# Performance work log

Measured on AMD Instinct MI355X. Metric: run time of the kernel, lower is better.

Reference implementation:

```python
import math
import jax, jax.numpy as jnp
import numpy as np

H, PQ, PV, E, C, S, N = 12, 4, 8, 16, 128, 384, 512


def setup_inputs() -> dict:
    key = jax.random.key(0)
    ks = jax.random.split(key, 16)
    rn = lambda k, shape, scale=1.0: jax.random.normal(k, shape, jnp.float32) * scale
    single = rn(ks[0], (N, S))
    pair = rn(ks[1], (N, N, C))
    R, _ = jnp.linalg.qr(rn(ks[2], (N, 3, 3)))  # proper orthonormal frames
    t = rn(ks[3], (N, 3))
    w = 0.02
    return dict(
        single_representation=single,
        pair_representation=pair,
        rotations=R,
        translations=t,
        Wq=rn(ks[4], (H, S, E), w),
        Wk=rn(ks[5], (H, S, E), w),
        Wv=rn(ks[6], (H, S, E), w),
        Wqp=rn(ks[7], (H, PQ, S, 3), w),
        Wkp=rn(ks[8], (H, PQ, S, 3), w),
        Wvp=rn(ks[9], (H, PV, S, 3), w),
        Wb=rn(ks[10], (H, C), w),
        Wout=rn(ks[11], (H * (C + E + PV * 4), S), w),
        b_out=jnp.zeros((S,), jnp.float32),
        scale_head=jnp.ones((H,), jnp.float32),
    )


def _frame_apply(R, t, pts):
    # R:[N,3,3], t:[N,3], pts:[H,P,N,3] -> R_n @ p + t_n per residue n
    return jnp.einsum('nij,hpnj->hpni', R, pts) + t[None, None, :, :]


def reference(single_representation, pair_representation, rotations, translations,
              Wq, Wk, Wv, Wqp, Wkp, Wvp, Wb, Wout, b_out, scale_head):
    single, pair = single_representation, pair_representation
    n = single.shape[0]

    # --- sequence QK term ---
    q = jnp.einsum('nd,hde->hne', single, Wq)
    k = jnp.einsum('nd,hde->hne', single, Wk)
    w_single = math.sqrt(1.0 / E) * jnp.einsum('hne,hme->hnm', q, k)  # [H,N,N]

    # --- pair bias term ---
    w_pair = jnp.einsum('nmc,hc->hnm', pair, Wb)  # [H,N,N]

    # --- frame (3D point distance) term ---
    qp = jnp.einsum('nd,hpdk->hpnk', single, Wqp)  # [H,PQ,N,3]
    kp = jnp.einsum('nd,hpdk->hpnk', single, Wkp)
    lqp = _frame_apply(rotations, translations, qp)
    lkp = _frame_apply(rotations, translations, kp)
    diff = lqp[:, :, :, None, :] - lkp[:, :, None, :, :]   # [H,PQ,N,N,3]
    sqd = jnp.sum(diff * diff, axis=(1, 4))                 # [H,N,N] (sum over points & xyz)
    w_frame = (-math.sqrt(1.0 / (18 * PQ))) * jax.nn.softplus(scale_head)[:, None, None] * sqd

    w = jax.nn.softmax(w_single + w_pair + w_frame, axis=-1)  # [H,N,N]

    # --- sequence value aggregation ---
    v = jnp.einsum('nd,hde->hne', single, Wv)
    att_single = jnp.einsum('hnm,hme->hne', w, v)             # [H,N,E]
    att_single = jnp.transpose(att_single, (1, 0, 2)).reshape(n, -1)

    # --- pair value aggregation (faithful to source: sums over query index too) ---
    colsum = jnp.sum(w, axis=1)                               # [H,N] = sum_a w[h,a,b]
    att_pair = jnp.einsum('hb,ibc->hic', colsum, pair)        # [H,N,C]
    att_pair = jnp.transpose(att_pair, (1, 0, 2)).reshape(n, -1)

    # --- 3D point value aggregation ---
    vp = jnp.einsum('nd,hpdk->hpnk', single, Wvp)             # [H,PV,N,3]
    lvp = _frame_apply(rotations, translations, vp)
    local_out = jnp.einsum('hnm,hpmk->hpnk', w, lvp)          # [H,PV,N,3]
    Rinv = jnp.swapaxes(rotations, -1, -2)                    # R^T
    tinv = -jnp.einsum('nij,nj->ni', Rinv, translations)      # -R^T t
    global_out = _frame_apply(Rinv, tinv, local_out)          # [H,PV,N,3]
    out_points = jnp.transpose(global_out, (2, 1, 0, 3)).reshape(n, -1)  # [N, PV*H*3]
    out_norm = jnp.linalg.norm(global_out, axis=-1)           # [H,PV,N]
    out_norm = jnp.transpose(out_norm, (2, 1, 0)).reshape(n, -1)         # [N, PV*H]

    att = jnp.concatenate([att_single, att_pair, out_points, out_norm], axis=-1)
    return att @ Wout + b_out
```

## Files before the change

### kernel.cpp

```cpp
#include <hip/hip_runtime.h>
#include <math.h>

#define NRES 512
#define HH 12
#define PQn 4
#define PVn 8
#define En 16
#define Cn 128
#define Sn 384
#define ATT_COLS 2112

#define OFF_Q    0
#define OFF_K    (OFF_Q   + HH*NRES*En)
#define OFF_V    (OFF_K   + HH*NRES*En)
#define OFF_LQP  (OFF_V   + HH*NRES*En)
#define OFF_LKP  (OFF_LQP + HH*NRES*12)
#define OFF_LVP  (OFF_LKP + HH*NRES*12)
#define OFF_CS   (OFF_LVP + HH*NRES*24)
#define OFF_ATT  (OFF_CS  + NRES*HH)
#define OFF_LG   (OFF_ATT + NRES*ATT_COLS)
#define OFF_PART OFF_LG
#define OFF_KC   OFF_ATT
#define OFF_D1   (OFF_KC + NRES*HH*28)
#define OFF_D0   (OFF_D1 + NRES*HH)
#define KSPLIT 16
#define KCHUNK (ATT_COLS/KSPLIT)
#define OROWS 8
#define NGRP 2

__global__ __launch_bounds__(256) void ipa_proj(
    const float* __restrict__ single, const float* __restrict__ Rm,
    const float* __restrict__ tr,
    const float* __restrict__ Wq, const float* __restrict__ Wk,
    const float* __restrict__ Wv, const float* __restrict__ Wqp,
    const float* __restrict__ Wkp, const float* __restrict__ Wvp,
    float* __restrict__ ws)
{
  float* q   = ws + OFF_Q;  float* k   = ws + OFF_K;  float* v   = ws + OFF_V;
  float* lqp = ws + OFF_LQP; float* lkp = ws + OFF_LKP; float* lvp = ws + OFF_LVP;
  const int n0 = blockIdx.x * 8;
  const int g  = blockIdx.y;
  const int tid = threadIdx.x;
  __shared__ float sS[8][388];
  __shared__ float sR[8][9];
  __shared__ float sT[8][3];
  #pragma unroll
  for (int i = 0; i < 3; ++i) {
    int idx = i*256 + tid;
    int r = idx / 96, c4 = idx % 96;
    float4 val = *reinterpret_cast<const float4*>(single + (size_t)(n0 + r)*Sn + c4*4);
    *reinterpret_cast<float4*>(&sS[r][c4*4]) = val;
  }
  if (tid < 72)      sR[tid/9][tid%9] = Rm[(size_t)(n0 + tid/9)*9 + tid%9];
  else if (tid < 96) { int r = (tid-72)/3; sT[r][(tid-72)%3] = tr[(size_t)(n0+r)*3 + (tid-72)%3]; }
  __syncthreads();
  #pragma unroll
  for (int i = 0; i < 3; ++i) {
    int item = i*256 + tid;
    int nl = item & 7;
    int ul = item >> 3;
    int u  = g*96 + ul;
    const float* srow = sS[nl];
    if (u < 576) {
      int which = u/192, r = u%192, h = r>>4, e = r&15;
      const float* W = (which==0 ? Wq : which==1 ? Wk : Wv) + (size_t)h*Sn*En + e;
      float acc = 0.f;
      #pragma unroll 8
      for (int d = 0; d < Sn; ++d) acc = fmaf(srow[d], W[(size_t)d*En], acc);
      float* dst = (which==0 ? q : which==1 ? k : v);
      dst[((size_t)h*NRES + (n0+nl))*En + e] = acc;
    } else {
      int u2 = u - 576;
      const float* W; float* dst;
      if (u2 < 48)      { int h=u2>>2,     p=u2&3;      W = Wqp + (size_t)(h*PQn+p)*Sn*3; dst = lqp + ((size_t)h*NRES + (n0+nl))*12 + p*3; }
      else if (u2 < 96) { int h=(u2-48)>>2,p=(u2-48)&3; W = Wkp + (size_t)(h*PQn+p)*Sn*3; dst = lkp + ((size_t)h*NRES + (n0+nl))*12 + p*3; }
      else              { int h=(u2-96)>>3,p=(u2-96)&7; W = Wvp + (size_t)(h*PVn+p)*Sn*3; dst = lvp + ((size_t)h*NRES + (n0+nl))*24 + p*3; }
      float x0=0.f,x1=0.f,x2=0.f;
      #pragma unroll 4
      for (int d = 0; d < Sn; ++d) {
        float sv = srow[d];
        x0 = fmaf(sv, W[d*3+0], x0);
        x1 = fmaf(sv, W[d*3+1], x1);
        x2 = fmaf(sv, W[d*3+2], x2);
      }
      const float* R8 = sR[nl]; const float* T8 = sT[nl];
      dst[0] = R8[0]*x0 + R8[1]*x1 + R8[2]*x2 + T8[0];
      dst[1] = R8[3]*x0 + R8[4]*x1 + R8[5]*x2 + T8[1];
      dst[2] = R8[6]*x0 + R8[7]*x1 + R8[8]*x2 + T8[2];
    }
  }
}

__global__ __launch_bounds__(256) void ipa_pack(
    const float* __restrict__ scale_head, float* __restrict__ ws)
{
  const float* k   = ws + OFF_K;
  const float* lkp = ws + OFF_LKP;
  const float* lqp = ws + OFF_LQP;
  float* kc = ws + OFF_KC;
  float* d1 = ws + OFF_D1;
  float* d0 = ws + OFF_D0;
  const int idx = blockIdx.x*256 + threadIdx.x;
  const int h = idx >> 9, m = idx & 511;
  const float gamma = 0.11785113019775793f * log1pf(__expf(scale_head[h]));
  const float* kr  = k   + ((size_t)h*NRES + m)*En;
  const float* lkr = lkp + ((size_t)h*NRES + m)*12;
  const float* lqr = lqp + ((size_t)h*NRES + m)*12;
  float* kcr = kc + ((size_t)m*HH + h)*28;
  #pragma unroll
  for (int e = 0; e < En; ++e) kcr[e] = 0.25f * kr[e];
  float Bm = 0.f, An = 0.f;
  #pragma unroll
  for (int j = 0; j < 12; ++j) {
    float b = lkr[j];
    kcr[16+j] = (2.f*gamma)*b;
    Bm = fmaf(b, b, Bm);
    float a = lqr[j];
    An = fmaf(a, a, An);
  }
  d1[m*HH + h] = -gamma*Bm;
  d0[m*HH + h] = -gamma*An;
}

__global__ __launch_bounds__(256) void ipa_logits(
    const float* __restrict__ pair, const float* __restrict__ Wb,
    float* __restrict__ ws)
{
  const float* q   = ws + OFF_Q;
  const float* lqp = ws + OFF_LQP;
  const float* kc  = ws + OFF_KC;
  const float* d1  = ws + OFF_D1;
  const float* d0  = ws + OFF_D0;
  float* lg = ws + OFF_LG;
  const int n0 = blockIdx.x * NGRP;
  const int m  = blockIdx.y * 256 + threadIdx.x;

  float acc[NGRP][HH];
  #pragma unroll
  for (int g = 0; g < NGRP; ++g)
    #pragma unroll
    for (int h = 0; h < HH; ++h) acc[g][h] = 0.f;

  const float4* prow0 = reinterpret_cast<const float4*>(pair + ((size_t)(n0+0)*NRES + m)*Cn);
  const float4* prow1 = reinterpret_cast<const float4*>(pair + ((size_t)(n0+1)*NRES + m)*Cn);
  #pragma unroll 4
  for (int c4 = 0; c4 < 32; ++c4) {
    float4 p0 = prow0[c4];
    float4 p1 = prow1[c4];
    #pragma unroll
    for (int h = 0; h < HH; ++h) {
      float4 wb = *reinterpret_cast<const float4*>(Wb + h*Cn + c4*4);
      acc[0][h] += p0.x*wb.x + p0.y*wb.y + p0.z*wb.z + p0.w*wb.w;
      acc[1][h] += p1.x*wb.x + p1.y*wb.y + p1.z*wb.z + p1.w*wb.w;
    }
  }

  float d1v[HH];
  {
    const float4* dd = reinterpret_cast<const float4*>(d1 + (size_t)m*HH);
    float4 a = dd[0], b = dd[1], c = dd[2];
    d1v[0]=a.x; d1v[1]=a.y; d1v[2]=a.z; d1v[3]=a.w;
    d1v[4]=b.x; d1v[5]=b.y; d1v[6]=b.z; d1v[7]=b.w;
    d1v[8]=c.x; d1v[9]=c.y; d1v[10]=c.z; d1v[11]=c.w;
  }

  const float* kcrow = kc + (size_t)m*HH*28;
  #pragma unroll
  for (int h = 0; h < HH; ++h) {
    const float4* kcr = reinterpret_cast<const float4*>(kcrow + h*28);
    float4 k0=kcr[0], k1=kcr[1], k2=kcr[2], k3=kcr[3], k4=kcr[4], k5=kcr[5], k6=kcr[6];
    #pragma unroll
    for (int g = 0; g < NGRP; ++g) {
      const int n = n0 + g;
      const float* qh  = q   + ((size_t)h*NRES + n)*En;
      const float* lqh = lqp + ((size_t)h*NRES + n)*12;
      float s = acc[g][h] + d1v[h] + d0[(size_t)n*HH + h];
      s += k0.x*qh[0]  + k0.y*qh[1]  + k0.z*qh[2]  + k0.w*qh[3];
      s += k1.x*qh[4]  + k1.y*qh[5]  + k1.z*qh[6]  + k1.w*qh[7];
      s += k2.x*qh[8]  + k2.y*qh[9]  + k2.z*qh[10] + k2.w*qh[11];
      s += k3.x*qh[12] + k3.y*qh[13] + k3.z*qh[14] + k3.w*qh[15];
      s += k4.x*lqh[0] + k4.y*lqh[1] + k4.z*lqh[2] + k4.w*lqh[3];
      s += k5.x*lqh[4] + k5.y*lqh[5] + k5.z*lqh[6] + k5.w*lqh[7];
      s += k6.x*lqh[8] + k6.y*lqh[9] + k6.z*lqh[10]+ k6.w*lqh[11];
      lg[((size_t)h*NRES + n)*NRES + m] = s;
    }
  }
}

__global__ __launch_bounds__(256) void ipa_softmax(float* __restrict__ ws)
{
  float* lg = ws + OFF_LG;
  const int row  = blockIdx.x*4 + (threadIdx.x >> 6);
  const int lane = threadIdx.x & 63;
  float4* p = reinterpret_cast<float4*>(lg + (size_t)row*NRES);
  float4 x0 = p[lane];
  float4 x1 = p[64 + lane];
  float mx = fmaxf(fmaxf(fmaxf(x0.x,x0.y),fmaxf(x0.z,x0.w)),
                   fmaxf(fmaxf(x1.x,x1.y),fmaxf(x1.z,x1.w)));
  #pragma unroll
  for (int off = 32; off >= 1; off >>= 1) mx = fmaxf(mx, __shfl_xor(mx, off));
  x0.x = __expf(x0.x-mx); x0.y = __expf(x0.y-mx); x0.z = __expf(x0.z-mx); x0.w = __expf(x0.w-mx);
  x1.x = __expf(x1.x-mx); x1.y = __expf(x1.y-mx); x1.z = __expf(x1.z-mx); x1.w = __expf(x1.w-mx);
  float sum = x0.x+x0.y+x0.z+x0.w + x1.x+x1.y+x1.z+x1.w;
  #pragma unroll
  for (int off = 32; off >= 1; off >>= 1) sum += __shfl_xor(sum, off);
  const float inv = 1.f/sum;
  x0.x*=inv; x0.y*=inv; x0.z*=inv; x0.w*=inv;
  x1.x*=inv; x1.y*=inv; x1.z*=inv; x1.w*=inv;
  p[lane] = x0;
  p[64 + lane] = x1;
}

__global__ __launch_bounds__(256) void ipa_colsum(float* __restrict__ ws)
{
  const float* lg = ws + OFF_LG;
  float* cs = ws + OFF_CS;
  const int h = blockIdx.x, ac = blockIdx.y, tid = threadIdx.x;
  const float* base = lg + (size_t)h*NRES*NRES + (size_t)ac*64*NRES;
  float acc0 = 0.f, acc1 = 0.f;
  #pragma unroll 4
  for (int a = 0; a < 64; ++a) {
    acc0 += base[(size_t)a*NRES + tid];
    acc1 += base[(size_t)a*NRES + tid + 256];
  }
  atomicAdd(&cs[h*NRES + tid],       acc0);
  atomicAdd(&cs[h*NRES + tid + 256], acc1);
}

__global__ __launch_bounds__(256) void ipa_agg(
    const float* __restrict__ Rm, const float* __restrict__ tr,
    float* __restrict__ ws)
{
  const float* v   = ws + OFF_V;
  const float* lvp = ws + OFF_LVP;
  const float* lg  = ws + OFF_LG;
  float* att = ws + OFF_ATT;
  const int row  = blockIdx.x*4 + (threadIdx.x >> 6);
  const int lane = threadIdx.x & 63;
  const int h = row >> 9, n = row & 511;

  float acc[40];
  #pragma unroll
  for (int i = 0; i < 40; ++i) acc[i] = 0.f;

  const float* wrow = lg + (size_t)row*NRES;
  #pragma unroll 2
  for (int j = 0; j < 8; ++j) {
    const int m = j*64 + lane;
    const float wv = wrow[m];
    const float4* v4 = reinterpret_cast<const float4*>(v + ((size_t)h*NRES + m)*En);
    float4 a0=v4[0], a1=v4[1], a2=v4[2], a3=v4[3];
    acc[0]+=wv*a0.x; acc[1]+=wv*a0.y; acc[2]+=wv*a0.z; acc[3]+=wv*a0.w;
    acc[4]+=wv*a1.x; acc[5]+=wv*a1.y; acc[6]+=wv*a1.z; acc[7]+=wv*a1.w;
    acc[8]+=wv*a2.x; acc[9]+=wv*a2.y; acc[10]+=wv*a2.z; acc[11]+=wv*a2.w;
    acc[12]+=wv*a3.x; acc[13]+=wv*a3.y; acc[14]+=wv*a3.z; acc[15]+=wv*a3.w;
    const float4* l4 = reinterpret_cast<const float4*>(lvp + ((size_t)h*NRES + m)*24);
    #pragma unroll
    for (int t = 0; t < 6; ++t) {
      float4 b = l4[t];
      acc[16+4*t+0]+=wv*b.x; acc[16+4*t+1]+=wv*b.y;
      acc[16+4*t+2]+=wv*b.z; acc[16+4*t+3]+=wv*b.w;
    }
  }
  #pragma unroll
  for (int off = 32; off >= 1; off >>= 1) {
    #pragma unroll
    for (int i = 0; i < 40; ++i) acc[i] += __shfl_xor(acc[i], off);
  }
  if (lane == 0) {
    size_t ab = (size_t)n*ATT_COLS;
    float4* as = reinterpret_cast<float4*>(att + ab + h*En);
    as[0] = make_float4(acc[0],acc[1],acc[2],acc[3]);
    as[1] = make_float4(acc[4],acc[5],acc[6],acc[7]);
    as[2] = make_float4(acc[8],acc[9],acc[10],acc[11]);
    as[3] = make_float4(acc[12],acc[13],acc[14],acc[15]);
    const float R0=Rm[n*9+0],R1=Rm[n*9+1],R2=Rm[n*9+2],
                R3=Rm[n*9+3],R4=Rm[n*9+4],R5=Rm[n*9+5],
                R6=Rm[n*9+6],R7=Rm[n*9+7],R8=Rm[n*9+8];
    const float t0=tr[n*3+0], t1=tr[n*3+1], t2=tr[n*3+2];
    #pragma unroll
    for (int pp = 0; pp < 8; ++pp) {
      float d0 = acc[16+3*pp+0]-t0, d1 = acc[16+3*pp+1]-t1, d2 = acc[16+3*pp+2]-t2;
      float g0 = R0*d0 + R3*d1 + R6*d2;
      float g1 = R1*d0 + R4*d1 + R7*d2;
      float g2 = R2*d0 + R5*d1 + R8*d2;
      att[ab + 1728 + (pp*HH + h)*3 + 0] = g0;
      att[ab + 1728 + (pp*HH + h)*3 + 1] = g1;
      att[ab + 1728 + (pp*HH + h)*3 + 2] = g2;
      att[ab + 2016 + pp*HH + h] = sqrtf(g0*g0 + g1*g1 + g2*g2);
    }
  }
}

__global__ __launch_bounds__(256) void ipa_pairagg(
    const float* __restrict__ pair, float* __restrict__ ws)
{
  const float* cs = ws + OFF_CS;
  float* att = ws + OFF_ATT;
  const int i = blockIdx.x, tid = threadIdx.x;
  __shared__ float sCS[HH*NRES];
  __shared__ float4 sRed[8][HH][32];
  #pragma unroll
  for (int it = 0; it < 6; ++it) {
    int idx = it*256 + tid;
    reinterpret_cast<float4*>(sCS)[idx] = reinterpret_cast<const float4*>(cs)[idx];
  }
  __syncthreads();
  const int c4 = tid & 31, bg = tid >> 5;
  float4 acc[HH];
  #pragma unroll
  for (int h = 0; h < HH; ++h) acc[h] = make_float4(0.f,0.f,0.f,0.f);
  const float* prow = pair + (size_t)i*NRES*Cn;
  for (int b = bg; b < NRES; b += 8) {
    float4 pv = *reinterpret_cast<const float4*>(prow + (size_t)b*Cn + c4*4);
    #pragma unroll
    for (int h = 0; h < HH; ++h) {
      float w = sCS[h*NRES + b];
      acc[h].x = fmaf(w, pv.x, acc[h].x);
      acc[h].y = fmaf(w, pv.y, acc[h].y);
      acc[h].z = fmaf(w, pv.z, acc[h].z);
      acc[h].w = fmaf(w, pv.w, acc[h].w);
    }
  }
  #pragma unroll
  for (int h = 0; h < HH; ++h) sRed[bg][h][c4] = acc[h];
  __syncthreads();
  for (int s = 4; s >= 1; s >>= 1) {
    if (bg < s) {
      #pragma unroll
      for (int h = 0; h < HH; ++h) {
        float4 a = sRed[bg][h][c4], b2 = sRed[bg+s][h][c4];
        a.x+=b2.x; a.y+=b2.y; a.z+=b2.z; a.w+=b2.w;
        sRed[bg][h][c4] = a;
      }
    }
    __syncthreads();
  }
  if (bg == 0) {
    size_t base = (size_t)i*ATT_COLS + 192;
    #pragma unroll
    for (int h = 0; h < HH; ++h)
      *reinterpret_cast<float4*>(att + base + h*Cn + c4*4) = sRed[0][h][c4];
  }
}

__global__ __launch_bounds__(384) void ipa_outp(
    const float* __restrict__ att, const float* __restrict__ Wout,
    float* __restrict__ ws)
{
  float* partial = ws + OFF_PART;
  const int rb = blockIdx.x;
  const int ks = blockIdx.y;
  const int s  = threadIdx.x;
  const int n0 = rb*OROWS;
  const int j0 = ks*KCHUNK;

  float acc[OROWS];
  #pragma unroll
  for (int r = 0; r < OROWS; ++r) acc[r] = 0.f;

  for (int jg = 0; jg < KCHUNK/4; ++jg) {
    const int j = j0 + jg*4;
    float w0 = Wout[(size_t)(j+0)*Sn + s];
    float w1 = Wout[(size_t)(j+1)*Sn + s];
    float w2 = Wout[(size_t)(j+2)*Sn + s];
    float w3 = Wout[(size_t)(j+3)*Sn + s];
    #pragma unroll
    for (int r = 0; r < OROWS; ++r) {
      float4 av = *reinterpret_cast<const float4*>(att + (size_t)(n0+r)*ATT_COLS + j);
      acc[r] = fmaf(av.x, w0, acc[r]);
      acc[r] = fmaf(av.y, w1, acc[r]);
      acc[r] = fmaf(av.z, w2, acc[r]);
      acc[r] = fmaf(av.w, w3, acc[r]);
    }
  }
  #pragma unroll
  for (int r = 0; r < OROWS; ++r)
    partial[((size_t)ks*NRES + n0 + r)*Sn + s] = acc[r];
}

__global__ __launch_bounds__(384) void ipa_outred(
    const float* __restrict__ b_out, float* __restrict__ ws,
    float* __restrict__ out)
{
  const float* partial = ws + OFF_PART;
  const int n = blockIdx.x, s = threadIdx.x;
  float a = b_out[s];
  #pragma unroll
  for (int ks = 0; ks < KSPLIT; ++ks)
    a += partial[((size_t)ks*NRES + n)*Sn + s];
  out[(size_t)n*Sn + s] = a;
}

extern "C" void kernel_launch(void* const* d_in, const int* in_sizes, int n_in,
                              void* d_out, int out_size, void* d_ws, size_t ws_size,
                              hipStream_t stream) {
  const float* single = (const float*)d_in[0];
  const float* pair   = (const float*)d_in[1];
  const float* Rm     = (const float*)d_in[2];
  const float* tr     = (const float*)d_in[3];
  const float* Wq     = (const float*)d_in[4];
  const float* Wk     = (const float*)d_in[5];
  const float* Wv     = (const float*)d_in[6];
  const float* Wqp    = (const float*)d_in[7];
  const float* Wkp    = (const float*)d_in[8];
  const float* Wvp    = (const float*)d_in[9];
  const float* Wb     = (const float*)d_in[10];
  const float* Wout   = (const float*)d_in[11];
  const float* b_out  = (const float*)d_in[12];
  const float* scale_head = (const float*)d_in[13];
  float* ws  = (float*)d_ws;
  float* out = (float*)d_out;

  hipMemsetAsync(ws + OFF_CS, 0, NRES*HH*sizeof(float), stream);
  ipa_proj   <<<dim3(64, 8),  256, 0, stream>>>(single, Rm, tr, Wq, Wk, Wv, Wqp, Wkp, Wvp, ws);
  ipa_pack   <<<dim3(24),     256, 0, stream>>>(scale_head, ws);
  ipa_logits <<<dim3(NRES/NGRP, NRES/256), 256, 0, stream>>>(pair, Wb, ws);
  ipa_softmax<<<dim3(HH*NRES/4), 256, 0, stream>>>(ws);
  ipa_colsum <<<dim3(HH, 8),  256, 0, stream>>>(ws);
  ipa_agg    <<<dim3(HH*NRES/4), 256, 0, stream>>>(Rm, tr, ws);
  ipa_pairagg<<<dim3(NRES),   256, 0, stream>>>(pair, ws);
  ipa_outp   <<<dim3(NRES/OROWS, KSPLIT), 384, 0, stream>>>(ws + OFF_ATT, Wout, ws);
  ipa_outred <<<dim3(NRES),   384, 0, stream>>>(b_out, ws, out);
}
```

Measured before the change: 265.3 us.

## Restructure logits to cache pair row in registers and repack colsum layout

The logits kernel now handles a single query row per block and loads all 128 pair channels into registers up front. It then loops over heads, using a packed q/point buffer that the pack kernel builds in the same layout as the key buffer. Colsum is stored transposed as [m][h], so pairagg can read the 12 head weights with float4 loads from shared memory. Pairagg also gives each warp a contiguous block of 64 keys and replaces the shared tree reduction with a shorter staged one. The 128-float register array and the launch bounds of 3 waves raise register pressure and may cause spills, and the logits grid doubles in block count.

```diff
diff --git a/kernel.cpp b/kernel.cpp
--- a/kernel.cpp
+++ b/kernel.cpp
@@ -23,10 +23,10 @@
 #define OFF_KC   OFF_ATT
 #define OFF_D1   (OFF_KC + NRES*HH*28)
 #define OFF_D0   (OFF_D1 + NRES*HH)
+#define OFF_QC   (OFF_D0 + NRES*HH)
 #define KSPLIT 16
 #define KCHUNK (ATT_COLS/KSPLIT)
 #define OROWS 8
-#define NGRP 2
 
 __global__ __launch_bounds__(256) void ipa_proj(
     const float* __restrict__ single, const float* __restrict__ Rm,
@@ -94,66 +94,54 @@
 __global__ __launch_bounds__(256) void ipa_pack(
     const float* __restrict__ scale_head, float* __restrict__ ws)
 {
+  const float* q   = ws + OFF_Q;
   const float* k   = ws + OFF_K;
   const float* lkp = ws + OFF_LKP;
   const float* lqp = ws + OFF_LQP;
   float* kc = ws + OFF_KC;
+  float* qc = ws + OFF_QC;
   float* d1 = ws + OFF_D1;
   float* d0 = ws + OFF_D0;
   const int idx = blockIdx.x*256 + threadIdx.x;
   const int h = idx >> 9, m = idx & 511;
   const float gamma = 0.11785113019775793f * log1pf(__expf(scale_head[h]));
   const float* kr  = k   + ((size_t)h*NRES + m)*En;
+  const float* qr  = q   + ((size_t)h*NRES + m)*En;
   const float* lkr = lkp + ((size_t)h*NRES + m)*12;
   const float* lqr = lqp + ((size_t)h*NRES + m)*12;
   float* kcr = kc + ((size_t)m*HH + h)*28;
-  #pragma unroll
-  for (int e = 0; e < En; ++e) kcr[e] = 0.25f * kr[e];
+  float* qcr = qc + ((size_t)m*HH + h)*28;
+  #pragma unroll
+  for (int e = 0; e < En; ++e) { kcr[e] = 0.25f * kr[e]; qcr[e] = qr[e]; }
   float Bm = 0.f, An = 0.f;
   #pragma unroll
   for (int j = 0; j < 12; ++j) {
-    float b = lkr[j];
+    float b = lkr[j], a = lqr[j];
     kcr[16+j] = (2.f*gamma)*b;
+    qcr[16+j] = a;
     Bm = fmaf(b, b, Bm);
-    float a = lqr[j];
     An = fmaf(a, a, An);
   }
   d1[m*HH + h] = -gamma*Bm;
   d0[m*HH + h] = -gamma*An;
 }
 
-__global__ __launch_bounds__(256) void ipa_logits(
+__global__ __launch_bounds__(256, 3) void ipa_logits(
     const float* __restrict__ pair, const float* __restrict__ Wb,
     float* __restrict__ ws)
 {
-  const float* q   = ws + OFF_Q;
-  const float* lqp = ws + OFF_LQP;
-  const float* kc  = ws + OFF_KC;
-  const float* d1  = ws + OFF_D1;
-  const float* d0  = ws + OFF_D0;
+  const float* kc = ws + OFF_KC;
+  const float* qc = ws + OFF_QC;
+  const float* d1 = ws + OFF_D1;
+  const float* d0 = ws + OFF_D0;
   float* lg = ws + OFF_LG;
-  const int n0 = blockIdx.x * NGRP;
-  const int m  = blockIdx.y * 256 + threadIdx.x;
-
-  float acc[NGRP][HH];
-  #pragma unroll
-  for (int g = 0; g < NGRP; ++g)
-    #pragma unroll
-    for (int h = 0; h < HH; ++h) acc[g][h] = 0.f;
-
-  const float4* prow0 = reinterpret_cast<const float4*>(pair + ((size_t)(n0+0)*NRES + m)*Cn);
-  const float4* prow1 = reinterpret_cast<const float4*>(pair + ((size_t)(n0+1)*NRES + m)*Cn);
-  #pragma unroll 4
-  for (int c4 = 0; c4 < 32; ++c4) {
-    float4 p0 = prow0[c4];
-    float4 p1 = prow1[c4];
-    #pragma unroll
-    for (int h = 0; h < HH; ++h) {
-      float4 wb = *reinterpret_cast<const float4*>(Wb + h*Cn + c4*4);
-      acc[0][h] += p0.x*wb.x + p0.y*wb.y + p0.z*wb.z + p0.w*wb.w;
-      acc[1][h] += p1.x*wb.x + p1.y*wb.y + p1.z*wb.z + p1.w*wb.w;
-    }
-  }
+  const int n = blockIdx.x;
+  const int m = blockIdx.y * 256 + threadIdx.x;
+
+  float4 row[32];
+  const float4* prow = reinterpret_cast<const float4*>(pair + ((size_t)n*NRES + m)*Cn);
+  #pragma unroll
+  for (int j = 0; j < 32; ++j) row[j] = prow[j];
 
   float d1v[HH];
   {
@@ -163,27 +151,29 @@
     d1v[4]=b.x; d1v[5]=b.y; d1v[6]=b.z; d1v[7]=b.w;
     d1v[8]=c.x; d1v[9]=c.y; d1v[10]=c.z; d1v[11]=c.w;
   }
-
   const float* kcrow = kc + (size_t)m*HH*28;
+  const float* qcrow = qc + (size_t)n*HH*28;
+  const float* d0row = d0 + (size_t)n*HH;
+
   #pragma unroll
   for (int h = 0; h < HH; ++h) {
     const float4* kcr = reinterpret_cast<const float4*>(kcrow + h*28);
-    float4 k0=kcr[0], k1=kcr[1], k2=kcr[2], k3=kcr[3], k4=kcr[4], k5=kcr[5], k6=kcr[6];
-    #pragma unroll
-    for (int g = 0; g < NGRP; ++g) {
-      const int n = n0 + g;
-      const float* qh  = q   + ((size_t)h*NRES + n)*En;
-      const float* lqh = lqp + ((size_t)h*NRES + n)*12;
-      float s = acc[g][h] + d1v[h] + d0[(size_t)n*HH + h];
-      s += k0.x*qh[0]  + k0.y*qh[1]  + k0.z*qh[2]  + k0.w*qh[3];
-      s += k1.x*qh[4]  + k1.y*qh[5]  + k1.z*qh[6]  + k1.w*qh[7];
-      s += k2.x*qh[8]  + k2.y*qh[9]  + k2.z*qh[10] + k2.w*qh[11];
-      s += k3.x*qh[12] + k3.y*qh[13] + k3.z*qh[14] + k3.w*qh[15];
-      s += k4.x*lqh[0] + k4.y*lqh[1] + k4.z*lqh[2] + k4.w*lqh[3];
-      s += k5.x*lqh[4] + k5.y*lqh[5] + k5.z*lqh[6] + k5.w*lqh[7];
-      s += k6.x*lqh[8] + k6.y*lqh[9] + k6.z*lqh[10]+ k6.w*lqh[11];
-      lg[((size_t)h*NRES + n)*NRES + m] = s;
-    }
+    const float4* qcr = reinterpret_cast<const float4*>(qcrow + h*28);
+    const float4* wbr = reinterpret_cast<const float4*>(Wb + h*Cn);
+    float s = d1v[h] + d0row[h];
+    #pragma unroll
+    for (int c4 = 0; c4 < 32; ++c4) {
+      float4 p = row[c4];
+      float4 w = wbr[c4];
+      s += p.x*w.x + p.y*w.y + p.z*w.z + p.w*w.w;
+    }
+    #pragma unroll
+    for (int j = 0; j < 7; ++j) {
+      float4 kv = kcr[j];
+      float4 qv = qcr[j];
+      s += kv.x*qv.x + kv.y*qv.y + kv.z*qv.z + kv.w*qv.w;
+    }
+    lg[((size_t)h*NRES + n)*NRES + m] = s;
   }
 }
 
@@ -223,8 +213,8 @@
     acc0 += base[(size_t)a*NRES + tid];
     acc1 += base[(size_t)a*NRES + tid + 256];
   }
-  atomicAdd(&cs[h*NRES + tid],       acc0);
-  atomicAdd(&cs[h*NRES + tid + 256], acc1);
+  atomicAdd(&cs[(size_t)tid*HH + h],       acc0);
+  atomicAdd(&cs[(size_t)(tid+256)*HH + h], acc1);
 }
 
 __global__ __launch_bounds__(256) void ipa_agg(
@@ -298,8 +288,8 @@
   const float* cs = ws + OFF_CS;
   float* att = ws + OFF_ATT;
   const int i = blockIdx.x, tid = threadIdx.x;
-  __shared__ float sCS[HH*NRES];
-  __shared__ float4 sRed[8][HH][32];
+  __shared__ float sCS[NRES*HH];
+  __shared__ float4 sRed[4][HH][32];
   #pragma unroll
   for (int it = 0; it < 6; ++it) {
     int idx = it*256 + tid;
@@ -307,40 +297,63 @@
   }
   __syncthreads();
   const int c4 = tid & 31, bg = tid >> 5;
+  const int b0 = bg * 64;
   float4 acc[HH];
   #pragma unroll
   for (int h = 0; h < HH; ++h) acc[h] = make_float4(0.f,0.f,0.f,0.f);
   const float* prow = pair + (size_t)i*NRES*Cn;
-  for (int b = bg; b < NRES; b += 8) {
-    float4 pv = *reinterpret_cast<const float4*>(prow + (size_t)b*Cn + c4*4);
-    #pragma unroll
-    for (int h = 0; h < HH; ++h) {
-      float w = sCS[h*NRES + b];
-      acc[h].x = fmaf(w, pv.x, acc[h].x);
-      acc[h].y = fmaf(w, pv.y, acc[h].y);
-      acc[h].z = fmaf(w, pv.z, acc[h].z);
-      acc[h].w = fmaf(w, pv.w, acc[h].w);
-    }
-  }
-  #pragma unroll
-  for (int h = 0; h < HH; ++h) sRed[bg][h][c4] = acc[h];
-  __syncthreads();
-  for (int s = 4; s >= 1; s >>= 1) {
-    if (bg < s) {
+  for (int jb = 0; jb < 64; jb += 4) {
+    float4 pv[4];
+    #pragma unroll
+    for (int u = 0; u < 4; ++u)
+      pv[u] = *reinterpret_cast<const float4*>(prow + (size_t)(b0+jb+u)*Cn + c4*4);
+    #pragma unroll
+    for (int u = 0; u < 4; ++u) {
+      const float4* csr = reinterpret_cast<const float4*>(&sCS[(b0+jb+u)*HH]);
+      float4 c0 = csr[0], c1 = csr[1], c2 = csr[2];
+      float w[12] = {c0.x,c0.y,c0.z,c0.w, c1.x,c1.y,c1.z,c1.w, c2.x,c2.y,c2.z,c2.w};
       #pragma unroll
       for (int h = 0; h < HH; ++h) {
-        float4 a = sRed[bg][h][c4], b2 = sRed[bg+s][h][c4];
-        a.x+=b2.x; a.y+=b2.y; a.z+=b2.z; a.w+=b2.w;
-        sRed[bg][h][c4] = a;
+        acc[h].x = fmaf(w[h], pv[u].x, acc[h].x);
+        acc[h].y = fmaf(w[h], pv[u].y, acc[h].y);
+        acc[h].z = fmaf(w[h], pv[u].z, acc[h].z);
+        acc[h].w = fmaf(w[h], pv[u].w, acc[h].w);
       }
     }
-    __syncthreads();
-  }
+  }
+  if (bg >= 4) {
+    for (int h = 0; h < HH; ++h) sRed[bg-4][h][c4] = acc[h];
+  }
+  __syncthreads();
+  if (bg < 4) {
+    for (int h = 0; h < HH; ++h) {
+      float4 b2 = sRed[bg][h][c4];
+      acc[h].x+=b2.x; acc[h].y+=b2.y; acc[h].z+=b2.z; acc[h].w+=b2.w;
+    }
+  }
+  __syncthreads();
+  if (bg >= 2 && bg < 4) {
+    for (int h = 0; h < HH; ++h) sRed[bg-2][h][c4] = acc[h];
+  }
+  __syncthreads();
+  if (bg < 2) {
+    for (int h = 0; h < HH; ++h) {
+      float4 b2 = sRed[bg][h][c4];
+      acc[h].x+=b2.x; acc[h].y+=b2.y; acc[h].z+=b2.z; acc[h].w+=b2.w;
+    }
+  }
+  __syncthreads();
+  if (bg == 1) {
+    for (int h = 0; h < HH; ++h) sRed[0][h][c4] = acc[h];
+  }
+  __syncthreads();
   if (bg == 0) {
     size_t base = (size_t)i*ATT_COLS + 192;
-    #pragma unroll
-    for (int h = 0; h < HH; ++h)
-      *reinterpret_cast<float4*>(att + base + h*Cn + c4*4) = sRed[0][h][c4];
+    for (int h = 0; h < HH; ++h) {
+      float4 b2 = sRed[0][h][c4];
+      acc[h].x+=b2.x; acc[h].y+=b2.y; acc[h].z+=b2.z; acc[h].w+=b2.w;
+      *reinterpret_cast<float4*>(att + base + h*Cn + c4*4) = acc[h];
+    }
   }
 }
 
@@ -415,7 +428,7 @@
   hipMemsetAsync(ws + OFF_CS, 0, NRES*HH*sizeof(float), stream);
   ipa_proj   <<<dim3(64, 8),  256, 0, stream>>>(single, Rm, tr, Wq, Wk, Wv, Wqp, Wkp, Wvp, ws);
   ipa_pack   <<<dim3(24),     256, 0, stream>>>(scale_head, ws);
-  ipa_logits <<<dim3(NRES/NGRP, NRES/256), 256, 0, stream>>>(pair, Wb, ws);
+  ipa_logits <<<dim3(NRES, 2), 256, 0, stream>>>(pair, Wb, ws);
   ipa_softmax<<<dim3(HH*NRES/4), 256, 0, stream>>>(ws);
   ipa_colsum <<<dim3(HH, 8),  256, 0, stream>>>(ws);
   ipa_agg    <<<dim3(HH*NRES/4), 256, 0, stream>>>(Rm, tr, ws);
```

New measurement: 281.9 us. 6.3% more time.
